# Performance work log

Measured on AMD Instinct MI355X. Metric: run time of the kernel, lower is better.

Reference implementation:

```python
import jax, jax.numpy as jnp
import numpy as np

B, C, N, T = 8, 256, 768, 12
HID = C // 4          # divided_hidden=4 -> hidden=64
HEADS = 1
D = HID // HEADS      # head_dim = 64
SCALE = D ** (-0.5)
EPS = 1e-6


def conv1x1(x, w, b):
    # x: [b,c,n,t], w: [o,c], b: [o]
    return jnp.einsum('bcnt,oc->bont', x, w) + b[:, None, None]


def layernorm_cf(x, w, b):
    # channels_first LayerNorm over axis 1
    u = x.mean(1, keepdims=True)
    s = ((x - u) ** 2).mean(1, keepdims=True)
    xh = (x - u) / jnp.sqrt(s + EPS)
    return w[:, None, None] * xh + b[:, None, None]


def setup_inputs() -> dict:
    key = jax.random.key(0)
    ks = jax.random.split(key, 32)
    f32 = jnp.float32
    inp = {
        'x': jax.random.normal(ks[0], (B, C, N, T), dtype=f32),
        'time_ind': jax.random.randint(ks[1], (B, T), 0, 288),
        'weekin': jax.random.randint(ks[2], (B, T), 0, 7),
        'holiin': jax.random.randint(ks[3], (B, T), 0, 2),
        'adj_s': jax.random.uniform(ks[4], (B, T, N, N), dtype=f32),
        'ln1_w': jnp.ones((C,), f32), 'ln1_b': jnp.zeros((C,), f32),
        'ln2_w': jnp.ones((C,), f32), 'ln2_b': jnp.zeros((C,), f32),
        'Wnq': jax.random.normal(ks[5], (C, HID), f32) * 0.05, 'bnq': jnp.zeros((HID,), f32),
        'Wnk': jax.random.normal(ks[6], (C, HID), f32) * 0.05, 'bnk': jnp.zeros((HID,), f32),
        'Wtq': jax.random.normal(ks[7], (C, HID), f32) * 0.05, 'btq': jnp.zeros((HID,), f32),
        'Wtk': jax.random.normal(ks[8], (C, HID), f32) * 0.05, 'btk': jnp.zeros((HID,), f32),
        'Bn': jax.random.normal(ks[9], (1, HEADS, N, N), f32) * 0.02,
        'Bt': jax.random.normal(ks[10], (1, HEADS, T, T), f32) * 0.02,
        'v_w': jax.random.normal(ks[11], (HID, C), f32) * 0.05, 'v_b': jnp.zeros((HID,), f32),
        'fcv_w': jax.random.normal(ks[12], (2 * HID, C), f32) * 0.05, 'fcv_b': jnp.zeros((2 * HID,), f32),
        'proj_w': jax.random.normal(ks[13], (C, 2 * HID), f32) * 0.05, 'proj_b': jnp.zeros((C,), f32),
        'ffn_w1': jax.random.normal(ks[14], (4 * C, C), f32) * 0.03, 'ffn_b1': jnp.zeros((4 * C,), f32),
        'ffn_w2': jax.random.normal(ks[15], (C, 2 * C), f32) * 0.03, 'ffn_b2': jnp.zeros((C,), f32),
    }
    return inp


def dual_axis(x, adj_s, Wnq, bnq, Wnk, bnk, Wtq, btq, Wtk, btk, Bn, Bt,
              v_w, v_b, fcv_w, fcv_b, proj_w, proj_b):
    # x: [b,f,n,t]; heads==1 so head dim folds into hidden.
    # --- node-axis attention ---
    xn = x.transpose(0, 3, 2, 1)                      # [b,t,n,f]
    nq = xn @ Wnq + bnq                               # [b,t,n,hid]
    nk = xn @ Wnk + bnk
    attn_n = jnp.einsum('btid,btjd->btij', nq, nk) * SCALE + Bn[0, 0]
    attn_n = jax.nn.softmax(attn_n, axis=-1) * adj_s  # [b,t,n,n]
    # --- time-axis attention ---
    xt = x.transpose(0, 2, 3, 1)                      # [b,n,t,f]
    tq = xt @ Wtq + btq                               # [b,n,t,hid]
    tk = xt @ Wtk + btk
    attn_t = jnp.einsum('bnid,bnjd->bnij', tq, tk) * SCALE + Bt[0, 0]
    attn_t = jax.nn.softmax(attn_t, axis=-1)          # [b,n,t,t]
    # --- values + nconv_2 aggregation ---
    v1 = conv1x1(x, v_w, v_b)                         # [b,hid,n,t]
    # sg: out[b,c,w,l] = sum_v v1[b,c,v,l] * attn_n[b,l,v,w]
    hs = jnp.einsum('bcvl,blvw->bcwl', v1, attn_n)    # [b,hid,n,t]
    # tg on time axis: v1 transposed to [b,hid,t,n]
    xtv = v1.transpose(0, 1, 3, 2)                    # [b,hid,t,n]
    tx = jnp.einsum('bcvl,blvw->bcwl', xtv, attn_t)   # [b,hid,t,n]
    ht = tx.transpose(0, 1, 3, 2)                     # [b,hid,n,t]
    h = jnp.concatenate([ht, hs], axis=1)             # [b,2hid,n,t]
    v = conv1x1(x, fcv_w, fcv_b)                      # [b,2hid,n,t]
    return conv1x1(h * v, proj_w, proj_b)             # [b,C,n,t]


def feedforward(x, w1, b1, w2, b2):
    y = conv1x1(x, w1, b1)                            # [b,4C,n,t]
    a, g = jnp.split(y, 2, axis=1)                    # each [b,2C,n,t]
    y = a * jax.nn.gelu(g, approximate=False)
    return conv1x1(y, w2, b2)


def reference(x, time_ind, weekin, holiin, adj_s,
              ln1_w, ln1_b, ln2_w, ln2_b,
              Wnq, bnq, Wnk, bnk, Wtq, btq, Wtk, btk, Bn, Bt,
              v_w, v_b, fcv_w, fcv_b, proj_w, proj_b,
              ffn_w1, ffn_b1, ffn_w2, ffn_b2):
    x1 = layernorm_cf(x, ln1_w, ln1_b)
    x = dual_axis(x1, adj_s, Wnq, bnq, Wnk, bnk, Wtq, btq, Wtk, btk, Bn, Bt,
                  v_w, v_b, fcv_w, fcv_b, proj_w, proj_b) + x
    x2 = layernorm_cf(x, ln2_w, ln2_b)
    x = feedforward(x2, ffn_w1, ffn_b1, ffn_w2, ffn_b2) + x
    return x
```

## Files before the change

### kernel.cpp

```cpp
#include <hip/hip_runtime.h>
#include <cstddef>

typedef unsigned short u16;
typedef __attribute__((ext_vector_type(8))) short bf16x8;
typedef __attribute__((ext_vector_type(4))) float f32x4;

constexpr int nB = 8, nC = 256, nN = 768, nT = 12, nM = nN * nT, nH = 64;
constexpr float SCALE = 0.125f;
constexpr float LNEPS = 1e-6f;

__device__ inline u16 f2b(float f) {
    union { float f; unsigned u; } v; v.f = f;
    unsigned r = v.u + 0x7FFFu + ((v.u >> 16) & 1u);
    return (u16)(r >> 16);
}
__device__ inline float b2f(u16 h) {
    union { unsigned u; float f; } v; v.u = ((unsigned)h) << 16;
    return v.f;
}
__device__ inline uint2 packb4(float a, float b, float c, float d) {
    uint2 r;
    r.x = (unsigned)f2b(a) | ((unsigned)f2b(b) << 16);
    r.y = (unsigned)f2b(c) | ((unsigned)f2b(d) << 16);
    return r;
}
__device__ inline f32x4 mfma16(bf16x8 a, bf16x8 b, f32x4 c) {
    return __builtin_amdgcn_mfma_f32_16x16x32_bf16(a, b, c, 0, 0, 0);
}

__device__ inline void stage64(const u16* __restrict__ g, int ld, u16* lds, int tid) {
#pragma unroll
    for (int r = 0; r < 2; ++r) {
        int c = tid + r * 256;
        int row = c >> 3, kc = (c & 7) * 8;
        *(uint4*)&lds[row * 72 + kc] = *(const uint4*)&g[(size_t)row * ld + kc];
    }
}

__device__ inline void mfma_block(const u16* As, const u16* Bs, f32x4 acc[2][2],
                                  int wo, int wm, int quad, int r) {
#pragma unroll
    for (int ks = 0; ks < 64; ks += 32) {
        bf16x8 a0 = *(const bf16x8*)&As[(wo + r) * 72 + ks + quad * 8];
        bf16x8 a1 = *(const bf16x8*)&As[(wo + 16 + r) * 72 + ks + quad * 8];
        bf16x8 b0 = *(const bf16x8*)&Bs[(wm + r) * 72 + ks + quad * 8];
        bf16x8 b1 = *(const bf16x8*)&Bs[(wm + 16 + r) * 72 + ks + quad * 8];
        acc[0][0] = mfma16(a0, b0, acc[0][0]);
        acc[0][1] = mfma16(a0, b1, acc[0][1]);
        acc[1][0] = mfma16(a1, b0, acc[1][0]);
        acc[1][1] = mfma16(a1, b1, acc[1][1]);
    }
}

__global__ __launch_bounds__(256) void cvt_w(const float* __restrict__ Wnq,
                                             const float* __restrict__ Wnk,
                                             const float* __restrict__ Wtq,
                                             const float* __restrict__ Wtk,
                                             const float* __restrict__ vw,
                                             const float* __restrict__ fcvw,
                                             const float* __restrict__ projw,
                                             const float* __restrict__ w1,
                                             const float* __restrict__ w2,
                                             u16* __restrict__ WB) {
    int i = blockIdx.x * 256 + threadIdx.x;
    float v;
    if (i < 65536) {
        int seg = i >> 14, j = i & 16383;
        int o = j >> 8, k = j & 255;
        const float* src = seg == 0 ? Wnq : seg == 1 ? Wnk : seg == 2 ? Wtq : Wtk;
        v = src[k * 64 + o];
    } else if (i < 81920)  v = vw[i - 65536];
    else if (i < 114688)   v = fcvw[i - 81920];
    else if (i < 147456)   v = projw[i - 114688];
    else if (i < 409600)   v = w1[i - 147456];
    else                   v = w2[i - 409600];
    WB[i] = f2b(v);
}

__global__ __launch_bounds__(256) void ln_cl(const float* __restrict__ X,
                                             const float* __restrict__ w,
                                             const float* __restrict__ bias,
                                             u16* __restrict__ Y) {
    int tid = threadIdx.x;
    int lane = tid & 63, cg = tid >> 6;
    int m0 = blockIdx.x * 64, b = blockIdx.y;
    size_t base = (size_t)b * nC * nM + m0 + lane;
    float s = 0.f, ss = 0.f;
#pragma unroll 4
    for (int k = 0; k < 64; ++k) {
        float v = X[base + (size_t)(cg * 64 + k) * nM];
        s += v; ss += v * v;
    }
    __shared__ float rs[4][64], rss[4][64], mu_s[64], rstd_s[64];
    __shared__ u16 Lo[64][264];
    rs[cg][lane] = s; rss[cg][lane] = ss;
    __syncthreads();
    if (tid < 64) {
        float t1 = rs[0][lane] + rs[1][lane] + rs[2][lane] + rs[3][lane];
        float t2 = rss[0][lane] + rss[1][lane] + rss[2][lane] + rss[3][lane];
        float mu = t1 * (1.f / nC);
        float var = t2 * (1.f / nC) - mu * mu;
        mu_s[lane] = mu;
        rstd_s[lane] = rsqrtf(var + LNEPS);
    }
    __syncthreads();
    float mu = mu_s[lane], rstd = rstd_s[lane];
#pragma unroll 8
    for (int k = 0; k < 64; k += 2) {
        int c = cg * 64 + k;
        float v0 = (X[base + (size_t)c * nM] - mu) * rstd * w[c] + bias[c];
        float v1 = (X[base + (size_t)(c + 1) * nM] - mu) * rstd * w[c + 1] + bias[c + 1];
        *(unsigned*)&Lo[lane][c] = (unsigned)f2b(v0) | ((unsigned)f2b(v1) << 16);
    }
    __syncthreads();
#pragma unroll
    for (int r = 0; r < 8; ++r) {
        int c = tid + r * 256;
        int mm = c >> 5, ch = (c & 31) * 8;
        *(uint4*)&Y[((size_t)b * nM + m0 + mm) * 256 + ch] = *(uint4*)&Lo[mm][ch];
    }
}

template <int COUT, int LAYOUT>
__global__ __launch_bounds__(256) void gemm_proj(const u16* __restrict__ X,
                                                 const u16* __restrict__ W,
                                                 const float* __restrict__ bias,
                                                 u16* __restrict__ OUT) {
    __shared__ u16 As[64 * 72], Bs[64 * 72];
    int tid = threadIdx.x;
    int m0 = blockIdx.x * 64, o0 = blockIdx.y * 64, b = blockIdx.z;
    int lane = tid & 63, wid = tid >> 6;
    int wo = (wid & 1) * 32, wm = (wid >> 1) * 32;
    int quad = lane >> 4, r = lane & 15;
    const u16* Ag = W + (size_t)o0 * 256;
    const u16* Bg = X + ((size_t)b * nM + m0) * 256;
    f32x4 acc[2][2] = {};
    for (int k0 = 0; k0 < 256; k0 += 64) {
        __syncthreads();
        stage64(Ag + k0, 256, As, tid);
        stage64(Bg + k0, 256, Bs, tid);
        __syncthreads();
        mfma_block(As, Bs, acc, wo, wm, quad, r);
    }
#pragma unroll
    for (int oi = 0; oi < 2; ++oi)
#pragma unroll
        for (int mj = 0; mj < 2; ++mj) {
            int o = o0 + wo + oi * 16 + quad * 4;
            int m = m0 + wm + mj * 16 + r;
            f32x4 a = acc[oi][mj];
            float v0 = a[0] + bias[o], v1 = a[1] + bias[o + 1];
            float v2 = a[2] + bias[o + 2], v3 = a[3] + bias[o + 3];
            if (LAYOUT == 1) {
                *(uint2*)&OUT[((size_t)b * nM + m) * COUT + o] = packb4(v0, v1, v2, v3);
            } else if (LAYOUT == 0) {
                int n = m / 12, t = m - n * 12;
                *(uint2*)&OUT[((size_t)(b * 12 + t) * nN + n) * COUT + o] =
                    packb4(v0, v1, v2, v3);
            } else {
                int n = m / 12, t = m - n * 12;
                size_t bt = (size_t)(b * 12 + t) * 64;
                OUT[(bt + o) * nN + n]     = f2b(v0);
                OUT[(bt + o + 1) * nN + n] = f2b(v1);
                OUT[(bt + o + 2) * nN + n] = f2b(v2);
                OUT[(bt + o + 3) * nN + n] = f2b(v3);
            }
        }
}

__global__ __launch_bounds__(256) void rowsum_k(const u16* __restrict__ NQ,
                                                const u16* __restrict__ NK,
                                                const float* __restrict__ Bn,
                                                float* __restrict__ RINV) {
    __shared__ u16 Qt[64 * 72], Kt[64 * 72];
    __shared__ float lsum[64];
    int tid = threadIdx.x;
    int i0 = blockIdx.x * 64, bt = blockIdx.y;
    int lane = tid & 63, wid = tid >> 6;
    int wo = (wid & 1) * 32, wm = (wid >> 1) * 32;
    int quad = lane >> 4, r = lane & 15;
    if (tid < 64) lsum[tid] = 0.f;
    stage64(NQ + ((size_t)bt * nN + i0) * 64, 64, Qt, tid);
    float rsm[2] = {0.f, 0.f};
    for (int j0 = 0; j0 < nN; j0 += 64) {
        __syncthreads();
        stage64(NK + ((size_t)bt * nN + j0) * 64, 64, Kt, tid);
        __syncthreads();
        f32x4 acc[2][2] = {};
        mfma_block(Kt, Qt, acc, wo, wm, quad, r);
#pragma unroll
        for (int mj = 0; mj < 2; ++mj) {
            int i_ = i0 + wm + mj * 16 + r;
#pragma unroll
            for (int oi = 0; oi < 2; ++oi) {
                int j_ = j0 + wo + oi * 16 + quad * 4;
                f32x4 b4 = *(const f32x4*)&Bn[(size_t)i_ * nN + j_];
#pragma unroll
                for (int rr = 0; rr < 4; ++rr)
                    rsm[mj] += expf(acc[oi][mj][rr] * SCALE + b4[rr]);
            }
        }
    }
#pragma unroll
    for (int mj = 0; mj < 2; ++mj) {
        rsm[mj] += __shfl_xor(rsm[mj], 16);
        rsm[mj] += __shfl_xor(rsm[mj], 32);
    }
    if (quad == 0) {
#pragma unroll
        for (int mj = 0; mj < 2; ++mj)
            atomicAdd(&lsum[wm + mj * 16 + r], rsm[mj]);
    }
    __syncthreads();
    if (tid < 64) RINV[(size_t)bt * nN + i0 + tid] = 1.f / lsum[tid];
}

__global__ __launch_bounds__(256) void node_agg_fused(const u16* __restrict__ NQ,
                                                      const u16* __restrict__ NK,
                                                      const u16* __restrict__ V1N,
                                                      const float* __restrict__ RINV,
                                                      const float* __restrict__ adj,
                                                      const float* __restrict__ Bn,
                                                      u16* __restrict__ HB) {
    __shared__ u16 Kt[64 * 72], Qt[64 * 72], Vt[64 * 72], Pt[64 * 72];
    __shared__ float rinv_s[64];
    int tid = threadIdx.x;
    int w0 = blockIdx.x * 64, bt = blockIdx.y;
    int b = bt / 12, l = bt - b * 12;
    int lane = tid & 63, wid = tid >> 6;
    int wo = (wid & 1) * 32, wm = (wid >> 1) * 32;
    int quad = lane >> 4, r = lane & 15;
    stage64(NK + ((size_t)bt * nN + w0) * 64, 64, Kt, tid);
    f32x4 acc2[2][2] = {};
    for (int v0 = 0; v0 < nN; v0 += 64) {
        __syncthreads();
        stage64(NQ + ((size_t)bt * nN + v0) * 64, 64, Qt, tid);
        stage64(V1N + (size_t)bt * 64 * nN + v0, nN, Vt, tid);
        if (tid < 64) rinv_s[tid] = RINV[(size_t)bt * nN + v0 + tid];
        __syncthreads();
        f32x4 acc1[2][2] = {};
        mfma_block(Kt, Qt, acc1, wo, wm, quad, r);
#pragma unroll
        for (int oi = 0; oi < 2; ++oi)
#pragma unroll
            for (int mj = 0; mj < 2; ++mj) {
                int wl = wo + oi * 16 + quad * 4;
                int vl = wm + mj * 16 + r;
                int v_ = v0 + vl;
                f32x4 a4 = *(const f32x4*)&adj[((size_t)bt * nN + v_) * nN + w0 + wl];
                f32x4 b4 = *(const f32x4*)&Bn[(size_t)v_ * nN + w0 + wl];
                float ri = rinv_s[vl];
#pragma unroll
                for (int rr = 0; rr < 4; ++rr) {
                    float e = expf(acc1[oi][mj][rr] * SCALE + b4[rr]) * a4[rr] * ri;
                    Pt[(wl + rr) * 72 + vl] = f2b(e);
                }
            }
        __syncthreads();
        mfma_block(Vt, Pt, acc2, wo, wm, quad, r);
    }
#pragma unroll
    for (int oi = 0; oi < 2; ++oi)
#pragma unroll
        for (int mj = 0; mj < 2; ++mj) {
            int c = wo + oi * 16 + quad * 4;
            int w = w0 + wm + mj * 16 + r;
            f32x4 a = acc2[oi][mj];
            *(uint2*)&HB[((size_t)b * nM + w * 12 + l) * 128 + 64 + c] =
                packb4(a[0], a[1], a[2], a[3]);
        }
}

__global__ __launch_bounds__(192) void time_attn(const u16* __restrict__ TQ,
                                                 const u16* __restrict__ TK,
                                                 const float* __restrict__ Bt,
                                                 float* __restrict__ AT) {
    int bn = blockIdx.x;
    __shared__ float tqs[nT * 64], tks[nT * 64], ss[nT * nT];
    __shared__ float inv_s[nT], max_s[nT];
    int tid = threadIdx.x;
    size_t base = (size_t)bn * nT * 64;
#pragma unroll
    for (int r = 0; r < 4; ++r) {
        int idx = tid + r * 192;
        tqs[idx] = b2f(TQ[base + idx]);
        tks[idx] = b2f(TK[base + idx]);
    }
    __syncthreads();
    if (tid < 144) {
        int i = tid / 12, j = tid % 12;
        float s = 0.f;
#pragma unroll
        for (int h = 0; h < 64; ++h) s += tqs[i * 64 + h] * tks[j * 64 + h];
        ss[tid] = s * SCALE + Bt[i * 12 + j];
    }
    __syncthreads();
    if (tid < 12) {
        float mx = -1e30f;
        for (int j = 0; j < 12; ++j) mx = fmaxf(mx, ss[tid * 12 + j]);
        float sm = 0.f;
        for (int j = 0; j < 12; ++j) sm += expf(ss[tid * 12 + j] - mx);
        max_s[tid] = mx; inv_s[tid] = 1.f / sm;
    }
    __syncthreads();
    if (tid < 144) {
        int i = tid / 12;
        AT[(size_t)bn * 144 + tid] = expf(ss[tid] - max_s[i]) * inv_s[i];
    }
}

__global__ __launch_bounds__(256) void time_agg_k(const u16* __restrict__ V1N,
                                                  const float* __restrict__ AT,
                                                  u16* __restrict__ HB) {
    int tid = threadIdx.x;
    int lane = tid & 63, cg = tid >> 6;
    int n = blockIdx.x * 64 + lane;
    int b = blockIdx.y;
    size_t bn = (size_t)b * nN + n;
#pragma unroll 2
    for (int cc = 0; cc < 16; ++cc) {
        int c = cg * 16 + cc;
        float acc[12] = {};
        for (int v = 0; v < 12; ++v) {
            float val = b2f(V1N[((size_t)(b * 12 + v) * 64 + c) * nN + n]);
            const float4* at4 = (const float4*)(AT + bn * 144 + v * 12);
            float4 a0 = at4[0], a1 = at4[1], a2 = at4[2];
            acc[0] += val * a0.x;  acc[1] += val * a0.y;
            acc[2] += val * a0.z;  acc[3] += val * a0.w;
            acc[4] += val * a1.x;  acc[5] += val * a1.y;
            acc[6] += val * a1.z;  acc[7] += val * a1.w;
            acc[8] += val * a2.x;  acc[9] += val * a2.y;
            acc[10] += val * a2.z; acc[11] += val * a2.w;
        }
#pragma unroll
        for (int t = 0; t < 12; ++t)
            HB[((size_t)b * nM + n * 12 + t) * 128 + c] = f2b(acc[t]);
    }
}

__global__ __launch_bounds__(256) void prodproj_k(const u16* __restrict__ HB,
                                                  const u16* __restrict__ VG,
                                                  const u16* __restrict__ W,
                                                  const float* __restrict__ bias,
                                                  const float* __restrict__ RES,
                                                  float* __restrict__ OUT) {
    __shared__ u16 As[64 * 72], Bs[64 * 72];
    int tid = threadIdx.x;
    int m0 = blockIdx.x * 64, o0 = blockIdx.y * 64, b = blockIdx.z;
    int lane = tid & 63, wid = tid >> 6;
    int wo = (wid & 1) * 32, wm = (wid >> 1) * 32;
    int quad = lane >> 4, r = lane & 15;
    f32x4 acc[2][2] = {};
    for (int k0 = 0; k0 < 128; k0 += 64) {
        __syncthreads();
        stage64(W + (size_t)o0 * 128 + k0, 128, As, tid);
#pragma unroll
        for (int rr = 0; rr < 2; ++rr) {
            int c = tid + rr * 256;
            int row = c >> 3, kc = (c & 7) * 8;
            size_t gi = ((size_t)b * nM + m0 + row) * 128 + k0 + kc;
            uint4 hv = *(const uint4*)&HB[gi];
            uint4 vv = *(const uint4*)&VG[gi];
            u16* hs = (u16*)&hv; u16* vs = (u16*)&vv;
            union { uint4 q; u16 s[8]; } ov;
#pragma unroll
            for (int q2 = 0; q2 < 8; ++q2) ov.s[q2] = f2b(b2f(hs[q2]) * b2f(vs[q2]));
            *(uint4*)&Bs[row * 72 + kc] = ov.q;
        }
        __syncthreads();
        mfma_block(As, Bs, acc, wo, wm, quad, r);
    }
#pragma unroll
    for (int oi = 0; oi < 2; ++oi)
#pragma unroll
        for (int mj = 0; mj < 2; ++mj) {
            int o = o0 + wo + oi * 16 + quad * 4;
            int m = m0 + wm + mj * 16 + r;
            f32x4 a = acc[oi][mj];
#pragma unroll
            for (int rr = 0; rr < 4; ++rr) {
                size_t idx = ((size_t)(b * nC + o + rr)) * nM + m;
                OUT[idx] = a[rr] + bias[o + rr] + RES[idx];
            }
        }
}

__global__ __launch_bounds__(256) void ffn1_k(const u16* __restrict__ X,
                                              const u16* __restrict__ W1,
                                              const float* __restrict__ B1,
                                              u16* __restrict__ G1) {
    __shared__ u16 As[64 * 72], Gs[64 * 72], Bs[64 * 72];
    int tid = threadIdx.x;
    int m0 = blockIdx.x * 64, o0 = blockIdx.y * 64, b = blockIdx.z;
    int lane = tid & 63, wid = tid >> 6;
    int wo = (wid & 1) * 32, wm = (wid >> 1) * 32;
    int quad = lane >> 4, r = lane & 15;
    f32x4 acca[2][2] = {}, accg[2][2] = {};
    for (int k0 = 0; k0 < 256; k0 += 64) {
        __syncthreads();
        stage64(W1 + (size_t)o0 * 256 + k0, 256, As, tid);
        stage64(W1 + (size_t)(512 + o0) * 256 + k0, 256, Gs, tid);
        stage64(X + ((size_t)b * nM + m0) * 256 + k0, 256, Bs, tid);
        __syncthreads();
#pragma unroll
        for (int ks = 0; ks < 64; ks += 32) {
            bf16x8 a0 = *(const bf16x8*)&As[(wo + r) * 72 + ks + quad * 8];
            bf16x8 a1 = *(const bf16x8*)&As[(wo + 16 + r) * 72 + ks + quad * 8];
            bf16x8 g0 = *(const bf16x8*)&Gs[(wo + r) * 72 + ks + quad * 8];
            bf16x8 g1 = *(const bf16x8*)&Gs[(wo + 16 + r) * 72 + ks + quad * 8];
            bf16x8 b0 = *(const bf16x8*)&Bs[(wm + r) * 72 + ks + quad * 8];
            bf16x8 b1 = *(const bf16x8*)&Bs[(wm + 16 + r) * 72 + ks + quad * 8];
            acca[0][0] = mfma16(a0, b0, acca[0][0]);
            acca[0][1] = mfma16(a0, b1, acca[0][1]);
            acca[1][0] = mfma16(a1, b0, acca[1][0]);
            acca[1][1] = mfma16(a1, b1, acca[1][1]);
            accg[0][0] = mfma16(g0, b0, accg[0][0]);
            accg[0][1] = mfma16(g0, b1, accg[0][1]);
            accg[1][0] = mfma16(g1, b0, accg[1][0]);
            accg[1][1] = mfma16(g1, b1, accg[1][1]);
        }
    }
#pragma unroll
    for (int oi = 0; oi < 2; ++oi)
#pragma unroll
        for (int mj = 0; mj < 2; ++mj) {
            int o = o0 + wo + oi * 16 + quad * 4;
            int m = m0 + wm + mj * 16 + r;
            float vals[4];
#pragma unroll
            for (int rr = 0; rr < 4; ++rr) {
                float aa = acca[oi][mj][rr] + B1[o + rr];
                float gg = accg[oi][mj][rr] + B1[512 + o + rr];
                float gl = 0.5f * gg * (1.f + erff(gg * 0.70710678118654752f));
                vals[rr] = aa * gl;
            }
            *(uint2*)&G1[((size_t)b * nM + m) * 512 + o] =
                packb4(vals[0], vals[1], vals[2], vals[3]);
        }
}

__global__ __launch_bounds__(256) void ffn2_k(const u16* __restrict__ G1,
                                              const u16* __restrict__ W2,
                                              const float* __restrict__ B2,
                                              const float* __restrict__ RES,
                                              float* __restrict__ OUT) {
    __shared__ u16 As[64 * 72], Bs[64 * 72];
    int tid = threadIdx.x;
    int m0 = blockIdx.x * 64, o0 = blockIdx.y * 64, b = blockIdx.z;
    int lane = tid & 63, wid = tid >> 6;
    int wo = (wid & 1) * 32, wm = (wid >> 1) * 32;
    int quad = lane >> 4, r = lane & 15;
    f32x4 acc[2][2] = {};
    for (int k0 = 0; k0 < 512; k0 += 64) {
        __syncthreads();
        stage64(W2 + (size_t)o0 * 512 + k0, 512, As, tid);
        stage64(G1 + ((size_t)b * nM + m0) * 512 + k0, 512, Bs, tid);
        __syncthreads();
        mfma_block(As, Bs, acc, wo, wm, quad, r);
    }
#pragma unroll
    for (int oi = 0; oi < 2; ++oi)
#pragma unroll
        for (int mj = 0; mj < 2; ++mj) {
            int o = o0 + wo + oi * 16 + quad * 4;
            int m = m0 + wm + mj * 16 + r;
            f32x4 a = acc[oi][mj];
#pragma unroll
            for (int rr = 0; rr < 4; ++rr) {
                size_t idx = ((size_t)(b * nC + o + rr)) * nM + m;
                OUT[idx] = a[rr] + B2[o + rr] + RES[idx];
            }
        }
}

extern "C" void kernel_launch(void* const* d_in, const int* in_sizes, int n_in,
                              void* d_out, int out_size, void* d_ws, size_t ws_size,
                              hipStream_t stream) {
    const float* x      = (const float*)d_in[0];
    const float* adj    = (const float*)d_in[4];
    const float* ln1w   = (const float*)d_in[5];
    const float* ln1b   = (const float*)d_in[6];
    const float* ln2w   = (const float*)d_in[7];
    const float* ln2b   = (const float*)d_in[8];
    const float* Wnq    = (const float*)d_in[9];
    const float* bnq    = (const float*)d_in[10];
    const float* Wnk    = (const float*)d_in[11];
    const float* bnk    = (const float*)d_in[12];
    const float* Wtq    = (const float*)d_in[13];
    const float* btq    = (const float*)d_in[14];
    const float* Wtk    = (const float*)d_in[15];
    const float* btk    = (const float*)d_in[16];
    const float* Bn     = (const float*)d_in[17];
    const float* Bt     = (const float*)d_in[18];
    const float* v_w    = (const float*)d_in[19];
    const float* v_b    = (const float*)d_in[20];
    const float* fcv_w  = (const float*)d_in[21];
    const float* fcv_b  = (const float*)d_in[22];
    const float* proj_w = (const float*)d_in[23];
    const float* proj_b = (const float*)d_in[24];
    const float* w1     = (const float*)d_in[25];
    const float* b1     = (const float*)d_in[26];
    const float* w2     = (const float*)d_in[27];
    const float* b2     = (const float*)d_in[28];
    float* out = (float*)d_out;

    char* p = (char*)d_ws;
    auto alloc = [&](size_t bytes) { char* q = p; p += (bytes + 255) & ~(size_t)255; return q; };
    u16*   x1cl   = (u16*)alloc(37748736);
    u16*   nqb    = (u16*)alloc(9437184);
    u16*   nkb    = (u16*)alloc(9437184);
    u16*   v1n    = (u16*)alloc(9437184);
    float* atT    = (float*)alloc(3538944);
    u16*   hb     = (u16*)alloc(18874368);
    u16*   vg     = (u16*)alloc(18874368);
    float* rinv   = (float*)alloc(294912);
    u16*   WB     = (u16*)alloc(1081344);
    float* xr     = (float*)alloc(75497472);
    u16*   x2cl   = (u16*)alloc(37748736);
    u16*   g1     = (u16*)alloc(75497472);

    dim3 blk(256);
    cvt_w<<<dim3(2112), blk, 0, stream>>>(Wnq, Wnk, Wtq, Wtk, v_w, fcv_w, proj_w,
                                          w1, w2, WB);
    ln_cl<<<dim3(144, nB), blk, 0, stream>>>(x, ln1w, ln1b, x1cl);
    gemm_proj<64, 0><<<dim3(144, 1, nB), blk, 0, stream>>>(x1cl, WB + 0, bnq, nqb);
    gemm_proj<64, 0><<<dim3(144, 1, nB), blk, 0, stream>>>(x1cl, WB + 16384, bnk, nkb);
    rowsum_k<<<dim3(12, nB * nT), blk, 0, stream>>>(nqb, nkb, Bn, rinv);
    gemm_proj<64, 2><<<dim3(144, 1, nB), blk, 0, stream>>>(x1cl, WB + 65536, v_b, v1n);
    node_agg_fused<<<dim3(12, nB * nT), blk, 0, stream>>>(nqb, nkb, v1n, rinv,
                                                          adj, Bn, hb);
    gemm_proj<64, 1><<<dim3(144, 1, nB), blk, 0, stream>>>(x1cl, WB + 32768, btq, nqb);
    gemm_proj<64, 1><<<dim3(144, 1, nB), blk, 0, stream>>>(x1cl, WB + 49152, btk, nkb);
    time_attn<<<dim3(nB * nN), dim3(192), 0, stream>>>(nqb, nkb, Bt, atT);
    time_agg_k<<<dim3(12, nB), blk, 0, stream>>>(v1n, atT, hb);
    gemm_proj<128, 1><<<dim3(144, 2, nB), blk, 0, stream>>>(x1cl, WB + 81920, fcv_b, vg);
    prodproj_k<<<dim3(144, 4, nB), blk, 0, stream>>>(hb, vg, WB + 114688, proj_b, x, xr);
    ln_cl<<<dim3(144, nB), blk, 0, stream>>>(xr, ln2w, ln2b, x2cl);
    ffn1_k<<<dim3(144, 8, nB), blk, 0, stream>>>(x2cl, WB + 147456, b1, g1);
    ffn2_k<<<dim3(144, 4, nB), blk, 0, stream>>>(g1, WB + 409600, b2, xr, out);
}
```

Before: 983.2 us.

## Software-pipeline node aggregation with register prefetch and double-buffered V tiles

Restructures the node_agg_fused loop so the next Q, V, RINV and adjacency tiles are loaded into registers while the current tile's scores and PV MFMA run. V now uses two LDS buffers, and the loop drops one barrier per iteration. The QK MFMA operands are swapped so each thread writes P as packed 4-element bf16 stores instead of scalar scattered stores. expf becomes __expf in both the row-sum and aggregation kernels. The cost is higher register pressure from the prefetched adjacency values and a full 12-iteration unroll, plus lower exp accuracy.

```diff
diff --git a/kernel.cpp b/kernel.cpp
--- a/kernel.cpp
+++ b/kernel.cpp
@@ -197,7 +197,7 @@
                 f32x4 b4 = *(const f32x4*)&Bn[(size_t)i_ * nN + j_];
 #pragma unroll
                 for (int rr = 0; rr < 4; ++rr)
-                    rsm[mj] += expf(acc[oi][mj][rr] * SCALE + b4[rr]);
+                    rsm[mj] += __expf(acc[oi][mj][rr] * SCALE + b4[rr]);
             }
         }
     }
@@ -222,7 +222,7 @@
                                                       const float* __restrict__ adj,
                                                       const float* __restrict__ Bn,
                                                       u16* __restrict__ HB) {
-    __shared__ u16 Kt[64 * 72], Qt[64 * 72], Vt[64 * 72], Pt[64 * 72];
+    __shared__ u16 Kt[64 * 72], Qt[64 * 72], Vta[64 * 72], Vtb[64 * 72], Pt[64 * 72];
     __shared__ float rinv_s[64];
     int tid = threadIdx.x;
     int w0 = blockIdx.x * 64, bt = blockIdx.y;
@@ -230,34 +230,102 @@
     int lane = tid & 63, wid = tid >> 6;
     int wo = (wid & 1) * 32, wm = (wid >> 1) * 32;
     int quad = lane >> 4, r = lane & 15;
+    int srow = tid >> 3, skc = (tid & 7) * 8;
+
+    const u16* Qg = NQ + (size_t)bt * nN * 64;
+    const u16* Vg = V1N + (size_t)bt * 64 * nN;
+    const float* Rg = RINV + (size_t)bt * nN;
+
     stage64(NK + ((size_t)bt * nN + w0) * 64, 64, Kt, tid);
+    stage64(Qg, 64, Qt, tid);
+    stage64(Vg, nN, Vta, tid);
+    if (tid < 64) rinv_s[tid] = Rg[tid];
+    float adjc[2][2][4];
+#pragma unroll
+    for (int oi = 0; oi < 2; ++oi)
+#pragma unroll
+        for (int mj = 0; mj < 2; ++mj) {
+            int vl = wo + oi * 16 + quad * 4;
+            int wl = w0 + wm + mj * 16 + r;
+#pragma unroll
+            for (int rr = 0; rr < 4; ++rr)
+                adjc[oi][mj][rr] = adj[((size_t)bt * nN + vl + rr) * nN + wl];
+        }
+    __syncthreads();
+
     f32x4 acc2[2][2] = {};
-    for (int v0 = 0; v0 < nN; v0 += 64) {
-        __syncthreads();
-        stage64(NQ + ((size_t)bt * nN + v0) * 64, 64, Qt, tid);
-        stage64(V1N + (size_t)bt * 64 * nN + v0, nN, Vt, tid);
-        if (tid < 64) rinv_s[tid] = RINV[(size_t)bt * nN + v0 + tid];
-        __syncthreads();
+    const u16* vcur = Vta;
+    u16* vnxt = Vtb;
+#pragma unroll
+    for (int i = 0; i < 12; ++i) {
+        int v0 = i * 64;
+        bool hn = i < 11;
+        uint4 qreg0 = {}, qreg1 = {}, vreg0 = {}, vreg1 = {};
+        float rreg = 0.f;
+        float adjn[2][2][4];
+        if (hn) {
+            int nv0 = v0 + 64;
+            qreg0 = *(const uint4*)&Qg[(size_t)(nv0 + srow) * 64 + skc];
+            qreg1 = *(const uint4*)&Qg[(size_t)(nv0 + srow + 32) * 64 + skc];
+            vreg0 = *(const uint4*)&Vg[(size_t)srow * nN + nv0 + skc];
+            vreg1 = *(const uint4*)&Vg[(size_t)(srow + 32) * nN + nv0 + skc];
+            if (tid < 64) rreg = Rg[nv0 + tid];
+#pragma unroll
+            for (int oi = 0; oi < 2; ++oi)
+#pragma unroll
+                for (int mj = 0; mj < 2; ++mj) {
+                    int vl = nv0 + wo + oi * 16 + quad * 4;
+                    int wl = w0 + wm + mj * 16 + r;
+#pragma unroll
+                    for (int rr = 0; rr < 4; ++rr)
+                        adjn[oi][mj][rr] = adj[((size_t)bt * nN + vl + rr) * nN + wl];
+                }
+        }
+        float bnc[2][2][4];
+#pragma unroll
+        for (int oi = 0; oi < 2; ++oi)
+#pragma unroll
+            for (int mj = 0; mj < 2; ++mj) {
+                int vl = v0 + wo + oi * 16 + quad * 4;
+                int wl = w0 + wm + mj * 16 + r;
+#pragma unroll
+                for (int rr = 0; rr < 4; ++rr)
+                    bnc[oi][mj][rr] = Bn[(size_t)(vl + rr) * nN + wl];
+            }
         f32x4 acc1[2][2] = {};
-        mfma_block(Kt, Qt, acc1, wo, wm, quad, r);
+        mfma_block(Qt, Kt, acc1, wo, wm, quad, r);
 #pragma unroll
         for (int oi = 0; oi < 2; ++oi)
 #pragma unroll
             for (int mj = 0; mj < 2; ++mj) {
-                int wl = wo + oi * 16 + quad * 4;
-                int vl = wm + mj * 16 + r;
-                int v_ = v0 + vl;
-                f32x4 a4 = *(const f32x4*)&adj[((size_t)bt * nN + v_) * nN + w0 + wl];
-                f32x4 b4 = *(const f32x4*)&Bn[(size_t)v_ * nN + w0 + wl];
-                float ri = rinv_s[vl];
+                int vl = wo + oi * 16 + quad * 4;
+                int wl = wm + mj * 16 + r;
+                float pv[4];
 #pragma unroll
                 for (int rr = 0; rr < 4; ++rr) {
-                    float e = expf(acc1[oi][mj][rr] * SCALE + b4[rr]) * a4[rr] * ri;
-                    Pt[(wl + rr) * 72 + vl] = f2b(e);
+                    float e = __expf(acc1[oi][mj][rr] * SCALE + bnc[oi][mj][rr]);
+                    pv[rr] = e * adjc[oi][mj][rr] * rinv_s[vl + rr];
                 }
+                *(uint2*)&Pt[wl * 72 + vl] = packb4(pv[0], pv[1], pv[2], pv[3]);
             }
         __syncthreads();
-        mfma_block(Vt, Pt, acc2, wo, wm, quad, r);
+        mfma_block(vcur, Pt, acc2, wo, wm, quad, r);
+        if (hn) {
+            *(uint4*)&Qt[srow * 72 + skc] = qreg0;
+            *(uint4*)&Qt[(srow + 32) * 72 + skc] = qreg1;
+            *(uint4*)&vnxt[srow * 72 + skc] = vreg0;
+            *(uint4*)&vnxt[(srow + 32) * 72 + skc] = vreg1;
+            if (tid < 64) rinv_s[tid] = rreg;
+#pragma unroll
+            for (int oi = 0; oi < 2; ++oi)
+#pragma unroll
+                for (int mj = 0; mj < 2; ++mj)
+#pragma unroll
+                    for (int rr = 0; rr < 4; ++rr)
+                        adjc[oi][mj][rr] = adjn[oi][mj][rr];
+        }
+        { const u16* t = vcur; vcur = vnxt; vnxt = (u16*)t; }
+        __syncthreads();
     }
 #pragma unroll
     for (int oi = 0; oi < 2; ++oi)
```

Result: faster. 926.0 us (-5.8%).
